# Performance work log

Measured on AMD Instinct MI355X. Metric: run time of the kernel, lower is better.

## Reference

```python
import jax, jax.numpy as jnp
import numpy as np

N_NODES = 100000
N_EDGES = 3200000
DIMS = [32, 256, 1024, 1024, 256, 6]


def setup_inputs() -> dict:
    key = jax.random.key(0)
    ks = jax.random.split(key, 2 + 2 * 5)
    inp = {
        "x": jax.random.normal(ks[0], (N_NODES, DIMS[0]), dtype=jnp.float32),
        "edge_index": jax.random.randint(ks[1], (2, N_EDGES), 0, N_NODES, dtype=jnp.int64),
    }
    for i in range(5):
        fan_in, fan_out = DIMS[i], DIMS[i + 1]
        scale = (2.0 / (fan_in + fan_out)) ** 0.5  # glorot-ish
        inp[f"W{i+1}"] = jax.random.normal(ks[2 + 2 * i], (fan_in, fan_out), dtype=jnp.float32) * scale
        inp[f"b{i+1}"] = jnp.zeros((fan_out,), dtype=jnp.float32)
    return inp


def _gcn_forward(x, edge_index, Ws, bs):
    N = x.shape[0]
    # add self loops (PyG GCNConv default)
    loop = jnp.arange(N, dtype=edge_index.dtype)
    src = jnp.concatenate([edge_index[0], loop])
    dst = jnp.concatenate([edge_index[1], loop])
    # symmetric normalization: deg computed on target index (gcn_norm)
    deg = jax.ops.segment_sum(jnp.ones_like(dst, dtype=x.dtype), dst, num_segments=N)
    dinv = jnp.where(deg > 0, jax.lax.rsqrt(deg), 0.0)
    norm = (dinv[src] * dinv[dst])[:, None]  # [E+N, 1]

    def conv(h, W, b):
        h = h @ W                                    # dense linear
        msg = h[src] * norm                          # gather + scale
        agg = jax.ops.segment_sum(msg, dst, num_segments=N)  # scatter-add
        return agg + b

    h = x
    for i in range(4):
        h = jax.nn.relu(conv(h, Ws[i], bs[i]))
    return conv(h, Ws[4], bs[4])


def reference(x, edge_index, W1, b1, W2, b2, W3, b3, W4, b4, W5, b5):
    return _gcn_forward(x, edge_index, (W1, W2, W3, W4, W5), (b1, b2, b3, b4, b5))
```

## Files before the change

### kernel.cpp

```cpp
#include <hip/hip_runtime.h>

typedef unsigned char u8;
typedef unsigned short u16;
typedef unsigned int u32;
typedef __bf16 bf16_t;
typedef bf16_t bf16x8 __attribute__((ext_vector_type(8)));
typedef float f32x4 __attribute__((ext_vector_type(4)));
typedef float f32x2 __attribute__((ext_vector_type(2)));

#define LDS_PTR(p) ((__attribute__((address_space(3))) unsigned int*)(p))
#define GLB_PTR(p) ((const __attribute__((address_space(1))) unsigned int*)(p))

#define BSH 9
#define BCAP 32768

static __device__ __forceinline__ float bf2f(u16 h) {
  u32 u = ((u32)h) << 16;
  return __builtin_bit_cast(float, u);
}
static __device__ __forceinline__ u16 f2bf(float f) {
  u32 u = __builtin_bit_cast(u32, f);
  u += 0x7fffu + ((u >> 16) & 1u);
  return (u16)(u >> 16);
}
static __device__ __forceinline__ void accum_d(float* acc, int j, u32 d, float w) {
  float lo = __builtin_bit_cast(float, d << 16);
  float hi = __builtin_bit_cast(float, d & 0xffff0000u);
  acc[j] += w * lo;
  acc[j + 1] += w * hi;
}

__global__ void detect_edge_kernel(const int* __restrict__ ei, int* __restrict__ flags) {
  __shared__ int nz;
  if (threadIdx.x == 0) nz = 0;
  __syncthreads();
  if (ei[1 + 2 * threadIdx.x] != 0) atomicAdd(&nz, 1);
  __syncthreads();
  if (threadIdx.x == 0) flags[0] = (nz == 0) ? 1 : 0;
}

__global__ void detect_x_kernel(const u16* __restrict__ x, int* __restrict__ flags) {
  __shared__ int cnt;
  if (threadIdx.x == 0) cnt = 0;
  __syncthreads();
  u32 u = x[threadIdx.x];
  u32 e = (u >> 7) & 0xFF;
  if (e >= 0x60 && e <= 0x83) atomicAdd(&cnt, 1);
  __syncthreads();
  if (threadIdx.x == 0) flags[1] = (cnt >= 240) ? 0 : 1;
}

static __device__ __forceinline__ int eidx(const void* ei, size_t i, int m) {
  return m ? (int)((const long long*)ei)[i] : ((const int*)ei)[i];
}

__global__ void zero_kernel(int* __restrict__ p, int n) {
  int i = blockIdx.x * 256 + threadIdx.x;
  if (i < n) p[i] = 0;
}

__global__ void zero_out_kernel(void* __restrict__ out, int n, const int* __restrict__ flags) {
  int i = blockIdx.x * 256 + threadIdx.x;
  if (i < n) {
    if (flags[1]) ((float*)out)[i] = 0.0f;
    else ((u16*)out)[i] = 0;
  }
}

__global__ void convert_w_kernel(const void* __restrict__ W, u16* __restrict__ Wt,
                                 int K, int N, int lgN, const int* __restrict__ flags) {
  int idx = blockIdx.x * 256 + threadIdx.x;
  if (idx < K * N) {
    int k, n;
    if (lgN >= 0) { k = idx >> lgN; n = idx & (N - 1); }
    else { k = idx / N; n = idx % N; }
    float v = flags[1] ? ((const float*)W)[idx] : bf2f(((const u16*)W)[idx]);
    Wt[n * K + k] = f2bf(v);
  }
}

__global__ __launch_bounds__(256) void bin_kernel(const void* __restrict__ ei,
                                                  int* __restrict__ gcur,
                                                  int2* __restrict__ pairs, int E, int Nn,
                                                  const int* __restrict__ flags, int nblk) {
  __shared__ int h[256];
  __shared__ int base[256];
  const int m = flags[0];
  const int nb = (Nn + (1 << BSH) - 1) >> BSH;
  const int per = (E + nblk - 1) / nblk;
  const int e0 = blockIdx.x * per;
  const int e1 = (e0 + per < E) ? e0 + per : E;
  for (int i = threadIdx.x; i < nb; i += 256) h[i] = 0;
  __syncthreads();
  for (int e = e0 + threadIdx.x; e < e1; e += 256) {
    int d = eidx(ei, (size_t)E + e, m);
    if ((u32)d < (u32)Nn) atomicAdd(&h[d >> BSH], 1);
  }
  __syncthreads();
  for (int i = threadIdx.x; i < nb; i += 256) {
    base[i] = atomicAdd(&gcur[i], h[i]);
    h[i] = 0;
  }
  __syncthreads();
  for (int e = e0 + threadIdx.x; e < e1; e += 256) {
    int d = eidx(ei, (size_t)E + e, m);
    if ((u32)d >= (u32)Nn) continue;
    int s = eidx(ei, (size_t)e, m);
    if ((u32)s >= (u32)Nn) s = 0;
    int b = d >> BSH;
    int p = base[b] + atomicAdd(&h[b], 1);
    if (p < BCAP) pairs[(size_t)b * BCAP + p] = make_int2(s, d);
  }
}

__global__ __launch_bounds__(256) void bucket_scan_kernel(const int* __restrict__ gcur,
                                                          int* __restrict__ gbase, int NB) {
  __shared__ int sd[256];
  int tid = threadIdx.x;
  int v = (tid < NB) ? gcur[tid] : 0;
  if (v > BCAP) v = BCAP;
  sd[tid] = v;
  __syncthreads();
  for (int s = 1; s < 256; s <<= 1) {
    int t = (tid >= s) ? sd[tid - s] : 0;
    __syncthreads();
    sd[tid] += t;
    __syncthreads();
  }
  if (tid < NB) gbase[tid] = sd[tid] - v;
}

__global__ __launch_bounds__(512) void bucket_finalize_kernel(
    const int2* __restrict__ pairs, const int* __restrict__ gcur,
    const int* __restrict__ gbase, int* __restrict__ rowp, float* __restrict__ dinv,
    int* __restrict__ csr, int Nn) {
  __shared__ int cnt[512];
  __shared__ int scn[512];
  const int b = blockIdx.x;
  const int n0 = b << BSH;
  const int tid = threadIdx.x;
  cnt[tid] = 0;
  __syncthreads();
  int tot = gcur[b];
  if (tot > BCAP) tot = BCAP;
  for (int i = tid; i < tot; i += 512) {
    int2 pr = pairs[(size_t)b * BCAP + i];
    atomicAdd(&cnt[pr.y - n0], 1);
  }
  __syncthreads();
  int myc = cnt[tid];
  scn[tid] = myc;
  __syncthreads();
  for (int s = 1; s < 512; s <<= 1) {
    int t = (tid >= s) ? scn[tid - s] : 0;
    __syncthreads();
    scn[tid] += t;
    __syncthreads();
  }
  const int node = n0 + tid;
  const int start = gbase[b] + scn[tid] - myc;
  if (node < Nn) {
    rowp[node] = start;
    dinv[node] = rsqrtf((float)(myc + 1));
    if (node == Nn - 1) rowp[Nn] = gbase[b] + scn[tid];
  }
  cnt[tid] = start;
  __syncthreads();
  for (int i = tid; i < tot; i += 512) {
    int2 pr = pairs[(size_t)b * BCAP + i];
    int p = atomicAdd(&cnt[pr.y - n0], 1);
    csr[p] = pr.x;
  }
}

template <int W, bool SRCF, bool DSTF>
__global__ __launch_bounds__(256) void spmm_kernel(
    const void* __restrict__ Hb, void* __restrict__ Gb,
    const int* __restrict__ rowp, const int* __restrict__ csr,
    const float* __restrict__ dinv, const u16* __restrict__ bias,
    int relu, int Nn, int src_stride, long long src_coloff,
    int dst_stride, long long dst_coloff, const int* __restrict__ flags) {
  constexpr int VPL = (W >= 64) ? (W / 64) : 1;
  constexpr int B = 16;
  const int lane = threadIdx.x & 63;
  const int node = __builtin_amdgcn_readfirstlane(blockIdx.x * 4 + (threadIdx.x >> 6));
  if (node >= Nn) return;
  const bool act = (W >= 64) || (lane < W);
  const int off = (W >= 64) ? lane * VPL : lane;
  int sf32 = 0, of32 = 0;
  if (SRCF) sf32 = flags[1];
  if (DSTF) of32 = flags[1];
  const u16* Hs = (const u16*)Hb;
  float acc[VPL];
#pragma unroll
  for (int j = 0; j < VPL; ++j) acc[j] = 0.0f;

  auto srcidx = [&](int s) -> size_t {
    return (size_t)src_coloff + (size_t)s * src_stride + off;
  };
  auto accum_row = [&](int s, float w) {
    if (!act) return;
    size_t idx = srcidx(s);
    if constexpr (W == 256) {
      int2 v = *(const int2*)(Hs + idx);
      accum_d(acc, 0, (u32)v.x, w);
      accum_d(acc, 2, (u32)v.y, w);
    } else {
      float val = (SRCF && sf32) ? ((const float*)Hb)[idx] : bf2f(Hs[idx]);
      acc[0] += w * val;
    }
  };

  const int e1 = rowp[node + 1];
  int e = rowp[node];

  for (; e + B <= e1; e += B) {
    int s[B];
#pragma unroll
    for (int j = 0; j < B; ++j) s[j] = csr[e + j];
    float wv[B];
#pragma unroll
    for (int j = 0; j < B; ++j) wv[j] = dinv[s[j]];
    if constexpr (W == 256) {
      int2 v[B];
#pragma unroll
      for (int j = 0; j < B; ++j) v[j] = *(const int2*)(Hs + srcidx(s[j]));
      if (act) {
#pragma unroll
        for (int j = 0; j < B; ++j) {
          accum_d(acc, 0, (u32)v[j].x, wv[j]);
          accum_d(acc, 2, (u32)v[j].y, wv[j]);
        }
      }
    } else {
      float v[B];
#pragma unroll
      for (int j = 0; j < B; ++j) {
        size_t idx = srcidx(s[j]);
        v[j] = (SRCF && sf32) ? ((const float*)Hb)[idx] : bf2f(Hs[idx]);
      }
      if (act) {
#pragma unroll
        for (int j = 0; j < B; ++j) acc[0] += wv[j] * v[j];
      }
    }
  }
  for (; e < e1; ++e) {
    int s = csr[e];
    accum_row(s, dinv[s]);
  }
  const float wi = dinv[node];
  accum_row(node, wi);
  if (!act) return;

  float vals[VPL];
#pragma unroll
  for (int j = 0; j < VPL; ++j) {
    float v = acc[j] * wi;
    if (bias) v += bf2f(bias[off + j]);
    if (relu) v = fmaxf(v, 0.0f);
    vals[j] = v;
  }
  size_t didx = (size_t)dst_coloff + (size_t)node * dst_stride + off;
  if constexpr (W == 256) {
    u32 d0 = (u32)f2bf(vals[0]) | ((u32)f2bf(vals[1]) << 16);
    u32 d1 = (u32)f2bf(vals[2]) | ((u32)f2bf(vals[3]) << 16);
    *(int2*)((u16*)Gb + didx) = make_int2((int)d0, (int)d1);
  } else {
    if (DSTF && of32) ((float*)Gb)[didx] = vals[0];
    else ((u16*)Gb)[didx] = f2bf(vals[0]);
  }
}

template <int W>
__global__ __launch_bounds__(256) void spmm_fp8_kernel(
    const u8* __restrict__ Hq, u16* __restrict__ Gout,
    const int* __restrict__ rowp, const int* __restrict__ csr,
    const float* __restrict__ dinv, int n0, int n1, int dst_stride) {
  constexpr int BPL = W / 64;
  constexpr int ND = BPL / 4;
  constexpr int B = (W == 1024) ? 8 : 16;
  const int lane = threadIdx.x & 63;
  const int node = __builtin_amdgcn_readfirstlane(n0 + blockIdx.x * 4 + (threadIdx.x >> 6));
  if (node >= n1) return;
  const int off = lane * BPL;
  f32x2 acc[2 * ND] = {};

  auto dec = [&](const u32* d, float w) {
    f32x2 w2 = {w, w};
#pragma unroll
    for (int q = 0; q < ND; ++q) {
      f32x2 a = __builtin_amdgcn_cvt_pk_f32_fp8((int)d[q], false);
      f32x2 b = __builtin_amdgcn_cvt_pk_f32_fp8((int)d[q], true);
      acc[2 * q] += w2 * a;
      acc[2 * q + 1] += w2 * b;
    }
  };

  const int e1r = rowp[node + 1];
  int e = rowp[node];
  for (; e + B <= e1r; e += B) {
    int s[B];
#pragma unroll
    for (int j = 0; j < B; ++j) s[j] = csr[e + j];
    float wv[B];
#pragma unroll
    for (int j = 0; j < B; ++j) wv[j] = dinv[s[j]];
    u32 v[B][ND];
#pragma unroll
    for (int j = 0; j < B; ++j) {
      const u8* p = Hq + (size_t)s[j] * W + off;
      if constexpr (ND == 4) *(int4*)&v[j][0] = *(const int4*)p;
      else v[j][0] = *(const u32*)p;
    }
#pragma unroll
    for (int j = 0; j < B; ++j) dec(v[j], wv[j]);
  }
  for (; e < e1r; ++e) {
    int s = csr[e];
    u32 v[ND];
    const u8* p = Hq + (size_t)s * W + off;
    if constexpr (ND == 4) *(int4*)&v[0] = *(const int4*)p;
    else v[0] = *(const u32*)p;
    dec(v, dinv[s]);
  }
  const float wi = dinv[node];
  {
    u32 v[ND];
    const u8* p = Hq + (size_t)node * W + off;
    if constexpr (ND == 4) *(int4*)&v[0] = *(const int4*)p;
    else v[0] = *(const u32*)p;
    dec(v, wi);
  }

  u32 d[2 * ND];
#pragma unroll
  for (int k = 0; k < 2 * ND; ++k) {
    float v0 = acc[k].x * wi, v1 = acc[k].y * wi;
    d[k] = (u32)f2bf(v0) | ((u32)f2bf(v1) << 16);
  }
  u16* gp = Gout + (size_t)(node - n0) * dst_stride + off;
  if constexpr (ND == 4) {
    ((int4*)gp)[0] = make_int4((int)d[0], (int)d[1], (int)d[2], (int)d[3]);
    ((int4*)gp)[1] = make_int4((int)d[4], (int)d[5], (int)d[6], (int)d[7]);
  } else {
    *(int2*)gp = make_int2((int)d[0], (int)d[1]);
  }
}

__global__ __launch_bounds__(256) void gemm_fast_kernel(
    const u16* __restrict__ A, int lda, const u16* __restrict__ Bt,
    u16* __restrict__ C, int ldc, const u16* __restrict__ bias,
    int M, int N, int K, int relu, int fp8out) {
  __shared__ __align__(16) u16 sA[128 * 64];
  __shared__ __align__(16) u16 sB[128 * 64];
  const int tid = threadIdx.x;
  const int lane = tid & 63;
  const int wave = __builtin_amdgcn_readfirstlane(tid >> 6);
  const int m0 = blockIdx.y * 128, n0 = blockIdx.x * 128;
  const int wm = (wave & 1) * 64, wn = (wave >> 1) * 64;
  const int lr = lane & 15, lq = lane >> 4;
  const int lrow = lane >> 3;
  const int lcol = (lane & 7) * 8;
  f32x4 acc[4][4] = {};

  for (int kb = 0; kb < K; kb += 64) {
#pragma unroll
    for (int it = 0; it < 4; ++it) {
      const int rbase = (it * 4 + wave) * 8;
      int gm = m0 + rbase + lrow;
      if (gm >= M) gm = M - 1;
      __builtin_amdgcn_global_load_lds(GLB_PTR(A + (size_t)gm * lda + kb + lcol),
                                       LDS_PTR(sA + rbase * 64), 16, 0, 0);
      const int gn = n0 + rbase + lrow;
      __builtin_amdgcn_global_load_lds(GLB_PTR(Bt + (size_t)gn * K + kb + lcol),
                                       LDS_PTR(sB + rbase * 64), 16, 0, 0);
    }
    __syncthreads();
#pragma unroll
    for (int ks = 0; ks < 2; ++ks) {
      bf16x8 af[4], bfr[4];
#pragma unroll
      for (int i = 0; i < 4; ++i)
        af[i] = *(const bf16x8*)(sA + (wm + i * 16 + lr) * 64 + ks * 32 + lq * 8);
#pragma unroll
      for (int i = 0; i < 4; ++i)
        bfr[i] = *(const bf16x8*)(sB + (wn + i * 16 + lr) * 64 + ks * 32 + lq * 8);
#pragma unroll
      for (int im = 0; im < 4; ++im)
#pragma unroll
        for (int in = 0; in < 4; ++in)
          acc[im][in] = __builtin_amdgcn_mfma_f32_16x16x32_bf16(af[im], bfr[in], acc[im][in], 0, 0, 0);
    }
    __syncthreads();
  }
#pragma unroll
  for (int im = 0; im < 4; ++im) {
#pragma unroll
    for (int in = 0; in < 4; ++in) {
      int col = n0 + wn + in * 16 + lr;
      float bv = bias ? bf2f(bias[col]) : 0.0f;
#pragma unroll
      for (int r = 0; r < 4; ++r) {
        int row = m0 + wm + im * 16 + lq * 4 + r;
        if (row < M) {
          float v = acc[im][in][r] + bv;
          if (relu) v = fmaxf(v, 0.0f);
          if (fp8out) {
            int pk = __builtin_amdgcn_cvt_pk_fp8_f32(v, v, 0, false);
            ((u8*)C)[(size_t)row * ldc + col] = (u8)(pk & 0xff);
          } else {
            C[(size_t)row * ldc + col] = f2bf(v);
          }
        }
      }
    }
  }
}

#define LP 72
__global__ __launch_bounds__(256) void gemm_small_kernel(
    const u16* __restrict__ A, int lda, const u16* __restrict__ Bt,
    u16* __restrict__ C, int ldc, const u16* __restrict__ bias,
    int M, int N, int K, int relu, int fp8out) {
  __shared__ __align__(16) u16 sA[128 * LP];
  __shared__ __align__(16) u16 sB[128 * LP];
  const int tid = threadIdx.x;
  const int lane = tid & 63, wave = tid >> 6;
  const int m0 = blockIdx.y * 128, n0 = blockIdx.x * 128;
  const int wm = (wave & 1) * 64, wn = (wave >> 1) * 64;
  const int lr = lane & 15;
  const int lq = lane >> 4;
  f32x4 acc[4][4] = {};

  for (int kb = 0; kb < K; kb += 64) {
#pragma unroll
    for (int it = 0; it < 4; ++it) {
      int linear = it * 2048 + tid * 8;
      int row = linear >> 6, kc = linear & 63;
      int gm = m0 + row, gk = kb + kc;
      int4 v = make_int4(0, 0, 0, 0);
      if (gm < M && gk < K) v = *(const int4*)(A + (size_t)gm * lda + gk);
      *(int4*)(sA + row * LP + kc) = v;
    }
#pragma unroll
    for (int it = 0; it < 4; ++it) {
      int linear = it * 2048 + tid * 8;
      int row = linear >> 6, kc = linear & 63;
      int gn = n0 + row, gk = kb + kc;
      int4 v = make_int4(0, 0, 0, 0);
      if (gn < N && gk < K) v = *(const int4*)(Bt + (size_t)gn * K + gk);
      *(int4*)(sB + row * LP + kc) = v;
    }
    __syncthreads();
#pragma unroll
    for (int ks = 0; ks < 2; ++ks) {
      bf16x8 af[4], bfr[4];
#pragma unroll
      for (int i = 0; i < 4; ++i)
        af[i] = *(const bf16x8*)(sA + (wm + i * 16 + lr) * LP + ks * 32 + lq * 8);
#pragma unroll
      for (int i = 0; i < 4; ++i)
        bfr[i] = *(const bf16x8*)(sB + (wn + i * 16 + lr) * LP + ks * 32 + lq * 8);
#pragma unroll
      for (int im = 0; im < 4; ++im)
#pragma unroll
        for (int in = 0; in < 4; ++in)
          acc[im][in] = __builtin_amdgcn_mfma_f32_16x16x32_bf16(af[im], bfr[in], acc[im][in], 0, 0, 0);
    }
    __syncthreads();
  }
#pragma unroll
  for (int im = 0; im < 4; ++im) {
#pragma unroll
    for (int in = 0; in < 4; ++in) {
      int col = n0 + wn + in * 16 + lr;
      if (col >= N) continue;
      float bv = bias ? bf2f(bias[col]) : 0.0f;
#pragma unroll
      for (int r = 0; r < 4; ++r) {
        int row = m0 + wm + im * 16 + lq * 4 + r;
        if (row < M) {
          float v = acc[im][in][r] + bv;
          if (relu) v = fmaxf(v, 0.0f);
          if (fp8out) {
            int pk = __builtin_amdgcn_cvt_pk_fp8_f32(v, v, 0, false);
            ((u8*)C)[(size_t)row * ldc + col] = (u8)(pk & 0xff);
          } else {
            C[(size_t)row * ldc + col] = f2bf(v);
          }
        }
      }
    }
  }
}

extern "C" void kernel_launch(void* const* d_in, const int* in_sizes, int n_in,
                              void* d_out, int out_size, void* d_ws, size_t ws_size,
                              hipStream_t stream) {
  const u16* x  = (const u16*)d_in[0];
  const int* ei = (const int*)d_in[1];

  const int Nn = in_sizes[0] / 32;
  const int E  = in_sizes[1] / 2;
  const int CH = (Nn + 7) / 8;
  const int NR = (Nn + CH - 1) / CH;
  const int NB = (Nn + (1 << BSH) - 1) >> BSH;

  char* w = (char*)d_ws;
  size_t off = 0;
  auto alloc = [&](size_t bytes) -> void* {
    void* p = w + off;
    off = (off + bytes + 255) & ~(size_t)255;
    return p;
  };
  int*   flags  = (int*)alloc(256);
  int*   gcur   = (int*)alloc(1024);
  int*   gbase  = (int*)alloc(1024);
  int*   rowp   = (int*)alloc((size_t)(Nn + 1) * 4);
  float* dinv   = (float*)alloc((size_t)Nn * 4);
  int*   csr    = (int*)alloc((size_t)E * 4);
  u16*   Wt1    = (u16*)alloc((size_t)32 * 256 * 2);
  u16*   Wt2    = (u16*)alloc((size_t)256 * 1024 * 2);
  u16*   Wt3    = (u16*)alloc((size_t)1024 * 1024 * 2);
  u16*   Wt4    = (u16*)alloc((size_t)1024 * 256 * 2);
  u16*   Wt5    = (u16*)alloc((size_t)256 * 6 * 2);
  u16*   bc1    = (u16*)alloc(256 * 2);
  u16*   bc2    = (u16*)alloc(1024 * 2);
  u16*   bc3    = (u16*)alloc(1024 * 2);
  u16*   bc4    = (u16*)alloc(256 * 2);
  u16*   bc5    = (u16*)alloc(6 * 2);
  size_t selems = (size_t)CH * 1024;
  u16*   S      = (u16*)alloc(selems * 2);
  u16*   H      = (u16*)alloc((size_t)Nn * 1024 * 2);
  const size_t required = off;
  (void)n_in;

  if (ws_size < required) {
    if (ws_size >= 4096) {
      detect_x_kernel<<<1, 256, 0, stream>>>(x, flags);
      zero_out_kernel<<<(out_size + 255) / 256, 256, 0, stream>>>(d_out, out_size, flags);
    }
    return;
  }

  u8*  h2q = (u8*)H;
  u16* g2  = H + (size_t)Nn * 512;
  u16* t4  = H + (size_t)Nn * 512;
  u8*  h1q = (u8*)(H + (size_t)Nn * 768);
  u16* h3R = H + (size_t)Nn * 768;
  u16* h4  = H + (size_t)Nn * 768;

  int2* pairs = (int2*)H;

  detect_edge_kernel<<<1, 256, 0, stream>>>(ei, flags);
  detect_x_kernel<<<1, 256, 0, stream>>>(x, flags);
  zero_kernel<<<1, 256, 0, stream>>>(gcur, 256);
  bin_kernel<<<1024, 256, 0, stream>>>(ei, gcur, pairs, E, Nn, flags, 1024);
  bucket_scan_kernel<<<1, 256, 0, stream>>>(gcur, gbase, NB);
  bucket_finalize_kernel<<<NB, 512, 0, stream>>>(pairs, gcur, gbase, rowp, dinv, csr, Nn);

  convert_w_kernel<<<(32 * 256 + 255) / 256, 256, 0, stream>>>(d_in[2], Wt1, 32, 256, 8, flags);
  convert_w_kernel<<<1, 256, 0, stream>>>(d_in[3], bc1, 1, 256, 8, flags);
  convert_w_kernel<<<(256 * 1024 + 255) / 256, 256, 0, stream>>>(d_in[4], Wt2, 256, 1024, 10, flags);
  convert_w_kernel<<<4, 256, 0, stream>>>(d_in[5], bc2, 1, 1024, 10, flags);
  convert_w_kernel<<<(1024 * 1024 + 255) / 256, 256, 0, stream>>>(d_in[6], Wt3, 1024, 1024, 10, flags);
  convert_w_kernel<<<4, 256, 0, stream>>>(d_in[7], bc3, 1, 1024, 10, flags);
  convert_w_kernel<<<(1024 * 256 + 255) / 256, 256, 0, stream>>>(d_in[8], Wt4, 1024, 256, 8, flags);
  convert_w_kernel<<<1, 256, 0, stream>>>(d_in[9], bc4, 1, 256, 8, flags);
  convert_w_kernel<<<(256 * 6 + 255) / 256, 256, 0, stream>>>(d_in[10], Wt5, 256, 6, -1, flags);
  convert_w_kernel<<<1, 256, 0, stream>>>(d_in[11], bc5, 1, 6, -1, flags);

  const int sg = (Nn + 3) / 4;
  const int mb = (Nn + 127) / 128;

  spmm_kernel<32, true, false><<<sg, 256, 0, stream>>>(x, S, rowp, csr, dinv, nullptr, 0, Nn,
                                                       32, 0, 32, 0, flags);
  gemm_small_kernel<<<dim3(2, mb), 256, 0, stream>>>(S, 32, Wt1, (u16*)h1q, 256, bc1,
                                                     Nn, 256, 32, 1, 1);

  spmm_fp8_kernel<256><<<sg, 256, 0, stream>>>(h1q, g2, rowp, csr, dinv, 0, Nn, 256);
  gemm_fast_kernel<<<dim3(8, mb), 256, 0, stream>>>(g2, 256, Wt2, (u16*)h2q, 1024, bc2,
                                                    Nn, 1024, 256, 1, 1);

  for (int R = 0; R < NR; ++R) {
    int n0 = R * CH;
    int n1 = n0 + CH < Nn ? n0 + CH : Nn;
    int MR = n1 - n0;
    int mbr = (MR + 127) / 128;
    spmm_fp8_kernel<1024><<<(MR + 3) / 4, 256, 0, stream>>>(h2q, S, rowp, csr, dinv, n0, n1, 1024);
    gemm_fast_kernel<<<dim3(8, mbr), 256, 0, stream>>>(S, 1024, Wt3, h3R, 1024, bc3,
                                                       MR, 1024, 1024, 1, 0);
    gemm_fast_kernel<<<dim3(2, mbr), 256, 0, stream>>>(h3R, 1024, Wt4, t4 + (size_t)n0 * 256, 256,
                                                       nullptr, MR, 256, 1024, 0, 0);
  }

  spmm_kernel<256, false, false><<<sg, 256, 0, stream>>>(
      H, H, rowp, csr, dinv, bc4, 1, Nn, 256, (long long)Nn * 512, 256, (long long)Nn * 768,
      flags);

  gemm_small_kernel<<<dim3(1, mb), 256, 0, stream>>>(h4, 256, Wt5, S, 6, nullptr,
                                                     Nn, 6, 256, 0, 0);
  spmm_kernel<6, false, true><<<sg, 256, 0, stream>>>(S, d_out, rowp, csr, dinv, bc5, 0, Nn,
                                                      6, 0, 6, 0, flags);
}
```

Before: 2.215 ms.

## Quantize layer-4 activations to int8 with global max scale before aggregation

The Wt4 GEMM now tracks a global absolute max of its output through a block reduction and an atomicMax. A new quant kernel packs t4 into int8 using that scale, and a new int8 SpMM kernel replaces the bf16 W=256 aggregation, halving the gather bytes per edge. The small detect kernels and the ten weight-conversion launches are each merged into a single launch. The change adds a quantization pass and a reduction epilogue, and per-tensor int8 loses precision.

```diff
diff --git a/kernel.cpp b/kernel.cpp
--- a/kernel.cpp
+++ b/kernel.cpp
@@ -30,24 +30,22 @@
   acc[j + 1] += w * hi;
 }
 
-__global__ void detect_edge_kernel(const int* __restrict__ ei, int* __restrict__ flags) {
-  __shared__ int nz;
-  if (threadIdx.x == 0) nz = 0;
-  __syncthreads();
-  if (ei[1 + 2 * threadIdx.x] != 0) atomicAdd(&nz, 1);
-  __syncthreads();
-  if (threadIdx.x == 0) flags[0] = (nz == 0) ? 1 : 0;
-}
-
-__global__ void detect_x_kernel(const u16* __restrict__ x, int* __restrict__ flags) {
+__global__ void detect_kernel(const int* __restrict__ ei, const u16* __restrict__ x,
+                              int* __restrict__ flags) {
   __shared__ int cnt;
   if (threadIdx.x == 0) cnt = 0;
   __syncthreads();
-  u32 u = x[threadIdx.x];
-  u32 e = (u >> 7) & 0xFF;
-  if (e >= 0x60 && e <= 0x83) atomicAdd(&cnt, 1);
-  __syncthreads();
-  if (threadIdx.x == 0) flags[1] = (cnt >= 240) ? 0 : 1;
+  if (blockIdx.x == 0) {
+    if (ei[1 + 2 * threadIdx.x] != 0) atomicAdd(&cnt, 1);
+    __syncthreads();
+    if (threadIdx.x == 0) flags[0] = (cnt == 0) ? 1 : 0;
+  } else {
+    u32 u = x[threadIdx.x];
+    u32 e = (u >> 7) & 0xFF;
+    if (e >= 0x60 && e <= 0x83) atomicAdd(&cnt, 1);
+    __syncthreads();
+    if (threadIdx.x == 0) flags[1] = (cnt >= 240) ? 0 : 1;
+  }
 }
 
 static __device__ __forceinline__ int eidx(const void* ei, size_t i, int m) {
@@ -67,15 +65,25 @@
   }
 }
 
-__global__ void convert_w_kernel(const void* __restrict__ W, u16* __restrict__ Wt,
-                                 int K, int N, int lgN, const int* __restrict__ flags) {
+struct CvtArgs {
+  const void* src[10];
+  u16* dst[10];
+  int K[10];
+  int N[10];
+  int start[11];
+};
+__global__ void convert_all_kernel(CvtArgs a, const int* __restrict__ flags) {
   int idx = blockIdx.x * 256 + threadIdx.x;
-  if (idx < K * N) {
-    int k, n;
-    if (lgN >= 0) { k = idx >> lgN; n = idx & (N - 1); }
-    else { k = idx / N; n = idx % N; }
-    float v = flags[1] ? ((const float*)W)[idx] : bf2f(((const u16*)W)[idx]);
-    Wt[n * K + k] = f2bf(v);
+  int f32 = flags[1];
+#pragma unroll
+  for (int t = 0; t < 10; ++t) {
+    if (idx >= a.start[t] && idx < a.start[t + 1]) {
+      int local = idx - a.start[t];
+      int K = a.K[t], N = a.N[t];
+      int k = local / N, n = local - k * N;
+      float v = f32 ? ((const float*)a.src[t])[local] : bf2f(((const u16*)a.src[t])[local]);
+      a.dst[t][(size_t)n * K + k] = f2bf(v);
+    }
   }
 }
 
@@ -180,40 +188,23 @@
     const float* __restrict__ dinv, const u16* __restrict__ bias,
     int relu, int Nn, int src_stride, long long src_coloff,
     int dst_stride, long long dst_coloff, const int* __restrict__ flags) {
-  constexpr int VPL = (W >= 64) ? (W / 64) : 1;
   constexpr int B = 16;
   const int lane = threadIdx.x & 63;
   const int node = __builtin_amdgcn_readfirstlane(blockIdx.x * 4 + (threadIdx.x >> 6));
   if (node >= Nn) return;
-  const bool act = (W >= 64) || (lane < W);
-  const int off = (W >= 64) ? lane * VPL : lane;
+  const bool act = lane < W;
+  const int off = lane;
   int sf32 = 0, of32 = 0;
   if (SRCF) sf32 = flags[1];
   if (DSTF) of32 = flags[1];
   const u16* Hs = (const u16*)Hb;
-  float acc[VPL];
-#pragma unroll
-  for (int j = 0; j < VPL; ++j) acc[j] = 0.0f;
+  float acc = 0.0f;
 
   auto srcidx = [&](int s) -> size_t {
     return (size_t)src_coloff + (size_t)s * src_stride + off;
   };
-  auto accum_row = [&](int s, float w) {
-    if (!act) return;
-    size_t idx = srcidx(s);
-    if constexpr (W == 256) {
-      int2 v = *(const int2*)(Hs + idx);
-      accum_d(acc, 0, (u32)v.x, w);
-      accum_d(acc, 2, (u32)v.y, w);
-    } else {
-      float val = (SRCF && sf32) ? ((const float*)Hb)[idx] : bf2f(Hs[idx]);
-      acc[0] += w * val;
-    }
-  };
-
   const int e1 = rowp[node + 1];
   int e = rowp[node];
-
   for (; e + B <= e1; e += B) {
     int s[B];
 #pragma unroll
@@ -221,55 +212,34 @@
     float wv[B];
 #pragma unroll
     for (int j = 0; j < B; ++j) wv[j] = dinv[s[j]];
-    if constexpr (W == 256) {
-      int2 v[B];
-#pragma unroll
-      for (int j = 0; j < B; ++j) v[j] = *(const int2*)(Hs + srcidx(s[j]));
-      if (act) {
-#pragma unroll
-        for (int j = 0; j < B; ++j) {
-          accum_d(acc, 0, (u32)v[j].x, wv[j]);
-          accum_d(acc, 2, (u32)v[j].y, wv[j]);
-        }
-      }
-    } else {
-      float v[B];
-#pragma unroll
-      for (int j = 0; j < B; ++j) {
-        size_t idx = srcidx(s[j]);
-        v[j] = (SRCF && sf32) ? ((const float*)Hb)[idx] : bf2f(Hs[idx]);
-      }
-      if (act) {
-#pragma unroll
-        for (int j = 0; j < B; ++j) acc[0] += wv[j] * v[j];
-      }
-    }
+    float v[B];
+#pragma unroll
+    for (int j = 0; j < B; ++j) {
+      size_t idx = srcidx(s[j]);
+      v[j] = act ? ((SRCF && sf32) ? ((const float*)Hb)[idx] : bf2f(Hs[idx])) : 0.0f;
+    }
+#pragma unroll
+    for (int j = 0; j < B; ++j) acc += wv[j] * v[j];
   }
   for (; e < e1; ++e) {
     int s = csr[e];
-    accum_row(s, dinv[s]);
+    if (act) {
+      size_t idx = srcidx(s);
+      acc += dinv[s] * ((SRCF && sf32) ? ((const float*)Hb)[idx] : bf2f(Hs[idx]));
+    }
   }
   const float wi = dinv[node];
-  accum_row(node, wi);
+  if (act) {
+    size_t idx = srcidx(node);
+    acc += wi * ((SRCF && sf32) ? ((const float*)Hb)[idx] : bf2f(Hs[idx]));
+  }
   if (!act) return;
-
-  float vals[VPL];
-#pragma unroll
-  for (int j = 0; j < VPL; ++j) {
-    float v = acc[j] * wi;
-    if (bias) v += bf2f(bias[off + j]);
-    if (relu) v = fmaxf(v, 0.0f);
-    vals[j] = v;
-  }
+  float v = acc * wi;
+  if (bias) v += bf2f(bias[off]);
+  if (relu) v = fmaxf(v, 0.0f);
   size_t didx = (size_t)dst_coloff + (size_t)node * dst_stride + off;
-  if constexpr (W == 256) {
-    u32 d0 = (u32)f2bf(vals[0]) | ((u32)f2bf(vals[1]) << 16);
-    u32 d1 = (u32)f2bf(vals[2]) | ((u32)f2bf(vals[3]) << 16);
-    *(int2*)((u16*)Gb + didx) = make_int2((int)d0, (int)d1);
-  } else {
-    if (DSTF && of32) ((float*)Gb)[didx] = vals[0];
-    else ((u16*)Gb)[didx] = f2bf(vals[0]);
-  }
+  if (DSTF && of32) ((float*)Gb)[didx] = v;
+  else ((u16*)Gb)[didx] = f2bf(v);
 }
 
 template <int W>
@@ -348,10 +318,83 @@
   }
 }
 
+__global__ __launch_bounds__(256) void spmm_i8_kernel(
+    const u8* __restrict__ Hq, u16* __restrict__ G,
+    const int* __restrict__ rowp, const int* __restrict__ csr,
+    const float* __restrict__ dinv, const u32* __restrict__ maxbits,
+    const u16* __restrict__ bias, int relu, int Nn, int dst_stride) {
+  constexpr int B = 16;
+  const int lane = threadIdx.x & 63;
+  const int node = __builtin_amdgcn_readfirstlane(blockIdx.x * 4 + (threadIdx.x >> 6));
+  if (node >= Nn) return;
+  const int off = lane * 4;
+  float mx = __builtin_bit_cast(float, *maxbits);
+  float sq = mx > 0.0f ? mx * (1.0f / 127.0f) : 0.0f;
+  float acc[4] = {};
+
+  auto dec = [&](u32 d, float w) {
+    acc[0] += w * (float)(int)(char)(d & 0xff);
+    acc[1] += w * (float)(int)(char)((d >> 8) & 0xff);
+    acc[2] += w * (float)(int)(char)((d >> 16) & 0xff);
+    acc[3] += w * (float)(int)(char)(d >> 24);
+  };
+
+  const int e1 = rowp[node + 1];
+  int e = rowp[node];
+  for (; e + B <= e1; e += B) {
+    int s[B];
+#pragma unroll
+    for (int j = 0; j < B; ++j) s[j] = csr[e + j];
+    float wv[B];
+#pragma unroll
+    for (int j = 0; j < B; ++j) wv[j] = dinv[s[j]];
+    u32 v[B];
+#pragma unroll
+    for (int j = 0; j < B; ++j) v[j] = *(const u32*)(Hq + (size_t)s[j] * 256 + off);
+#pragma unroll
+    for (int j = 0; j < B; ++j) dec(v[j], wv[j]);
+  }
+  for (; e < e1; ++e) {
+    int s = csr[e];
+    dec(*(const u32*)(Hq + (size_t)s * 256 + off), dinv[s]);
+  }
+  const float wi = dinv[node];
+  dec(*(const u32*)(Hq + (size_t)node * 256 + off), wi);
+
+  float vals[4];
+#pragma unroll
+  for (int k = 0; k < 4; ++k) {
+    float v = acc[k] * wi * sq;
+    if (bias) v += bf2f(bias[off + k]);
+    if (relu) v = fmaxf(v, 0.0f);
+    vals[k] = v;
+  }
+  u32 d0 = (u32)f2bf(vals[0]) | ((u32)f2bf(vals[1]) << 16);
+  u32 d1 = (u32)f2bf(vals[2]) | ((u32)f2bf(vals[3]) << 16);
+  *(int2*)(G + (size_t)node * dst_stride + off) = make_int2((int)d0, (int)d1);
+}
+
+__global__ void quant_kernel(const u16* __restrict__ t4, u8* __restrict__ t4q,
+                             const u32* __restrict__ maxbits, int n4) {
+  int i = blockIdx.x * 256 + threadIdx.x;
+  if (i >= n4) return;
+  float mx = __builtin_bit_cast(float, *maxbits);
+  float inv = mx > 0.0f ? 127.0f / mx : 0.0f;
+  int2 v = ((const int2*)t4)[i];
+  float f0 = bf2f((u16)(v.x & 0xffff)), f1 = bf2f((u16)((u32)v.x >> 16));
+  float f2 = bf2f((u16)(v.y & 0xffff)), f3 = bf2f((u16)((u32)v.y >> 16));
+  int q0 = (int)rintf(f0 * inv), q1 = (int)rintf(f1 * inv);
+  int q2 = (int)rintf(f2 * inv), q3 = (int)rintf(f3 * inv);
+  q0 = min(127, max(-127, q0)); q1 = min(127, max(-127, q1));
+  q2 = min(127, max(-127, q2)); q3 = min(127, max(-127, q3));
+  ((u32*)t4q)[i] = (u32)(q0 & 0xff) | ((u32)(q1 & 0xff) << 8) |
+                   ((u32)(q2 & 0xff) << 16) | ((u32)(q3 & 0xff) << 24);
+}
+
 __global__ __launch_bounds__(256) void gemm_fast_kernel(
     const u16* __restrict__ A, int lda, const u16* __restrict__ Bt,
     u16* __restrict__ C, int ldc, const u16* __restrict__ bias,
-    int M, int N, int K, int relu, int fp8out) {
+    int M, int N, int K, int relu, int fp8out, u32* __restrict__ maxout) {
   __shared__ __align__(16) u16 sA[128 * 64];
   __shared__ __align__(16) u16 sB[128 * 64];
   const int tid = threadIdx.x;
@@ -394,6 +437,7 @@
     }
     __syncthreads();
   }
+  u32 mymax = 0;
 #pragma unroll
   for (int im = 0; im < 4; ++im) {
 #pragma unroll
@@ -406,6 +450,10 @@
         if (row < M) {
           float v = acc[im][in][r] + bv;
           if (relu) v = fmaxf(v, 0.0f);
+          if (maxout) {
+            u32 ab = __builtin_bit_cast(u32, v) & 0x7fffffffu;
+            mymax = mymax > ab ? mymax : ab;
+          }
           if (fp8out) {
             int pk = __builtin_amdgcn_cvt_pk_fp8_f32(v, v, 0, false);
             ((u8*)C)[(size_t)row * ldc + col] = (u8)(pk & 0xff);
@@ -415,6 +463,16 @@
         }
       }
     }
+  }
+  if (maxout) {
+    u32* red = (u32*)sA;
+    red[tid] = mymax;
+    __syncthreads();
+    for (int s = 128; s > 0; s >>= 1) {
+      if (tid < s) red[tid] = red[tid] > red[tid + s] ? red[tid] : red[tid + s];
+      __syncthreads();
+    }
+    if (tid == 0) atomicMax(maxout, red[0]);
   }
 }
 
@@ -517,6 +575,7 @@
   int*   flags  = (int*)alloc(256);
   int*   gcur   = (int*)alloc(1024);
   int*   gbase  = (int*)alloc(1024);
+  u32*   tmax   = (u32*)alloc(256);
   int*   rowp   = (int*)alloc((size_t)(Nn + 1) * 4);
   float* dinv   = (float*)alloc((size_t)Nn * 4);
   int*   csr    = (int*)alloc((size_t)E * 4);
@@ -538,13 +597,14 @@
 
   if (ws_size < required) {
     if (ws_size >= 4096) {
-      detect_x_kernel<<<1, 256, 0, stream>>>(x, flags);
+      detect_kernel<<<2, 256, 0, stream>>>(ei, x, flags);
       zero_out_kernel<<<(out_size + 255) / 256, 256, 0, stream>>>(d_out, out_size, flags);
     }
     return;
   }
 
   u8*  h2q = (u8*)H;
+  u8*  t4q = (u8*)H;
   u16* g2  = H + (size_t)Nn * 512;
   u16* t4  = H + (size_t)Nn * 512;
   u8*  h1q = (u8*)(H + (size_t)Nn * 768);
@@ -553,23 +613,29 @@
 
   int2* pairs = (int2*)H;
 
-  detect_edge_kernel<<<1, 256, 0, stream>>>(ei, flags);
-  detect_x_kernel<<<1, 256, 0, stream>>>(x, flags);
-  zero_kernel<<<1, 256, 0, stream>>>(gcur, 256);
+  detect_kernel<<<2, 256, 0, stream>>>(ei, x, flags);
+  zero_kernel<<<3, 256, 0, stream>>>(gcur, 576);
   bin_kernel<<<1024, 256, 0, stream>>>(ei, gcur, pairs, E, Nn, flags, 1024);
   bucket_scan_kernel<<<1, 256, 0, stream>>>(gcur, gbase, NB);
   bucket_finalize_kernel<<<NB, 512, 0, stream>>>(pairs, gcur, gbase, rowp, dinv, csr, Nn);
 
-  convert_w_kernel<<<(32 * 256 + 255) / 256, 256, 0, stream>>>(d_in[2], Wt1, 32, 256, 8, flags);
-  convert_w_kernel<<<1, 256, 0, stream>>>(d_in[3], bc1, 1, 256, 8, flags);
-  convert_w_kernel<<<(256 * 1024 + 255) / 256, 256, 0, stream>>>(d_in[4], Wt2, 256, 1024, 10, flags);
-  convert_w_kernel<<<4, 256, 0, stream>>>(d_in[5], bc2, 1, 1024, 10, flags);
-  convert_w_kernel<<<(1024 * 1024 + 255) / 256, 256, 0, stream>>>(d_in[6], Wt3, 1024, 1024, 10, flags);
-  convert_w_kernel<<<4, 256, 0, stream>>>(d_in[7], bc3, 1, 1024, 10, flags);
-  convert_w_kernel<<<(1024 * 256 + 255) / 256, 256, 0, stream>>>(d_in[8], Wt4, 1024, 256, 8, flags);
-  convert_w_kernel<<<1, 256, 0, stream>>>(d_in[9], bc4, 1, 256, 8, flags);
-  convert_w_kernel<<<(256 * 6 + 255) / 256, 256, 0, stream>>>(d_in[10], Wt5, 256, 6, -1, flags);
-  convert_w_kernel<<<1, 256, 0, stream>>>(d_in[11], bc5, 1, 6, -1, flags);
+  {
+    CvtArgs a;
+    const int Ks[10] = {32, 1, 256, 1, 1024, 1, 1024, 1, 256, 1};
+    const int Ns[10] = {256, 256, 1024, 1024, 1024, 1024, 256, 256, 6, 6};
+    u16* ds[10] = {Wt1, bc1, Wt2, bc2, Wt3, bc3, Wt4, bc4, Wt5, bc5};
+    int cum = 0;
+    for (int t = 0; t < 10; ++t) {
+      a.src[t] = d_in[2 + t];
+      a.dst[t] = ds[t];
+      a.K[t] = Ks[t];
+      a.N[t] = Ns[t];
+      a.start[t] = cum;
+      cum += Ks[t] * Ns[t];
+    }
+    a.start[10] = cum;
+    convert_all_kernel<<<(cum + 255) / 256, 256, 0, stream>>>(a, flags);
+  }
 
   const int sg = (Nn + 3) / 4;
   const int mb = (Nn + 127) / 128;
@@ -581,7 +647,7 @@
 
   spmm_fp8_kernel<256><<<sg, 256, 0, stream>>>(h1q, g2, rowp, csr, dinv, 0, Nn, 256);
   gemm_fast_kernel<<<dim3(8, mb), 256, 0, stream>>>(g2, 256, Wt2, (u16*)h2q, 1024, bc2,
-                                                    Nn, 1024, 256, 1, 1);
+                                                    Nn, 1024, 256, 1, 1, nullptr);
 
   for (int R = 0; R < NR; ++R) {
     int n0 = R * CH;
@@ -590,14 +656,14 @@
     int mbr = (MR + 127) / 128;
     spmm_fp8_kernel<1024><<<(MR + 3) / 4, 256, 0, stream>>>(h2q, S, rowp, csr, dinv, n0, n1, 1024);
     gemm_fast_kernel<<<dim3(8, mbr), 256, 0, stream>>>(S, 1024, Wt3, h3R, 1024, bc3,
-                                                       MR, 1024, 1024, 1, 0);
+                                                       MR, 1024, 1024, 1, 0, nullptr);
     gemm_fast_kernel<<<dim3(2, mbr), 256, 0, stream>>>(h3R, 1024, Wt4, t4 + (size_t)n0 * 256, 256,
-                                                       nullptr, MR, 256, 1024, 0, 0);
-  }
-
-  spmm_kernel<256, false, false><<<sg, 256, 0, stream>>>(
-      H, H, rowp, csr, dinv, bc4, 1, Nn, 256, (long long)Nn * 512, 256, (long long)Nn * 768,
-      flags);
+                                                       nullptr, MR, 256, 1024, 0, 0, tmax);
+  }
+
+  quant_kernel<<<(Nn * 64 + 255) / 256, 256, 0, stream>>>(t4, t4q, tmax, Nn * 64);
+
+  spmm_i8_kernel<<<sg, 256, 0, stream>>>(t4q, h4, rowp, csr, dinv, tmax, bc4, 1, Nn, 256);
 
   gemm_small_kernel<<<dim3(1, mb), 256, 0, stream>>>(h4, 256, Wt5, S, 6, nullptr,
                                                      Nn, 6, 256, 0, 0);
```

New measurement: 2.186 ms. No clear change (-1.3%).
